# Kernel optimization log

Hardware: AMD Instinct MI355X
Metric: run time of the kernel (lower is better)

## Reference

```python
import jax, jax.numpy as jnp
import numpy as np

N_NODES = 100000
N_EDGES = 3200000
IN_FEATS = 512
HIDDEN = 256
N_CLASSES = 64
NITER = 10
HALT_BIAS_INIT = 3.0


def setup_inputs() -> dict:
    key = jax.random.key(0)
    ks = jax.random.split(key, 8)
    x = jax.random.normal(ks[0], (N_NODES, IN_FEATS), dtype=jnp.float32)
    edge_index = jax.random.randint(ks[1], (2, N_EDGES), 0, N_NODES, dtype=jnp.int64)
    # Linear layers: layers[0]: in->hidden, layers[1]: hidden->classes, halt: classes->1
    W0 = jax.random.normal(ks[2], (IN_FEATS, HIDDEN), dtype=jnp.float32) / np.sqrt(IN_FEATS)
    b0 = jnp.zeros((HIDDEN,), dtype=jnp.float32)
    W1 = jax.random.normal(ks[3], (HIDDEN, N_CLASSES), dtype=jnp.float32) / np.sqrt(HIDDEN)
    b1 = jnp.zeros((N_CLASSES,), dtype=jnp.float32)
    Wh = jax.random.normal(ks[4], (N_CLASSES, 1), dtype=jnp.float32) / np.sqrt(N_CLASSES)
    bh = jnp.full((1,), HALT_BIAS_INIT, dtype=jnp.float32)
    return {"x": x, "edge_index": edge_index, "edge_dropout": 0,
            "W0": W0, "b0": b0, "W1": W1, "b1": b1, "Wh": Wh, "bh": bh}


def reference(x, edge_index, edge_dropout, W0, b0, W1, b1, Wh, bh):
    N = x.shape[0]
    # MLP encoder (eval mode: dropout is identity)
    h = jax.nn.relu(x @ W0 + b0)
    h = h @ W1 + b1                                   # [N, C]

    # gcn_norm with self-loops (edge_dropout=0 in eval => identical every iter)
    loops = jnp.arange(N, dtype=edge_index.dtype)
    row = jnp.concatenate([edge_index[0], loops])     # source
    col = jnp.concatenate([edge_index[1], loops])     # target (aggregation index)
    deg = jax.ops.segment_sum(jnp.ones_like(col, dtype=h.dtype), col, num_segments=N)
    dinv = jnp.where(deg > 0, deg ** -0.5, 0.0)
    norm = dinv[row] * dinv[col]                      # [E+N]

    def step(ph, _):
        msg = norm[:, None] * ph[row]                 # gather + scale, [E+N, C]
        ph2 = jax.ops.segment_sum(msg, col, num_segments=N)  # scatter_add
        logit = jnp.clip(ph2 @ Wh + bh, -10.0, 10.0)  # [N, 1]
        return ph2, (ph2, logit)

    _, (props, logits) = jax.lax.scan(step, h, None, length=NITER)
    outputs = jnp.concatenate([h[None], props], axis=0)       # [niter+1, N, C]
    halting_logits = jnp.transpose(logits[:, :, 0])           # [N, niter]

    lam = jax.nn.sigmoid(halting_logits)
    remain = jnp.cumprod(1.0 - lam, axis=1)                   # inclusive
    remain_excl = jnp.concatenate([jnp.ones((N, 1), lam.dtype), remain[:, :-1]], axis=1)
    p = lam * remain_excl
    p = p.at[:, -1].add(remain[:, -1])                        # leftover mass to last step
    return outputs, p, halting_logits
```

## Files before the change

### kernel.cpp

```cpp
#include <hip/hip_runtime.h>
#include <hip/hip_bf16.h>

#define N_NODES  100000
#define N_EDGES  3200000
#define IN_FEATS 512
#define HIDDEN   256
#define N_CLASSES 64
#define NITER    10

#define SCAN_NB  49

#define OUT_P_OFF  ((size_t)(NITER + 1) * N_NODES * N_CLASSES)
#define OUT_HL_OFF (OUT_P_OFF + (size_t)N_NODES * NITER)

#define WS_META_INTS (4 * N_NODES + 128)
#define WS_CSR_OFF   ((size_t)WS_META_INTS * 4)
#define WS_W0F_OFF   (WS_CSR_OFF + (size_t)2 * N_EDGES * 4)
#define WS_W1F_OFF   (WS_W0F_OFF + 262144)
#define WS_SH0_OFF   (WS_W1F_OFF + 32768)
#define WS_SH1_OFF   (WS_SH0_OFF + (size_t)N_NODES * 64 * 2)
#define WS_NEED_W    (WS_SH0_OFF)
#define WS_NEED_BF   (WS_SH1_OFF + (size_t)N_NODES * 64 * 2)

typedef _Float16 f16x8 __attribute__((ext_vector_type(8)));
typedef _Float16 f16x4 __attribute__((ext_vector_type(4)));
typedef float    f32x4 __attribute__((ext_vector_type(4)));

__device__ __forceinline__ float bflo(unsigned v) { return __uint_as_float(v << 16); }
__device__ __forceinline__ float bfhi(unsigned v) { return __uint_as_float(v & 0xffff0000u); }
__device__ __forceinline__ unsigned short f2bf(float f) {
    unsigned u = __float_as_uint(f);
    return (unsigned short)((u + 0x7fffu + ((u >> 16) & 1u)) >> 16);
}

__global__ void k_detect(const int* ei, int* flag) {
    if (threadIdx.x == 0 && blockIdx.x == 0) {
        int is64 = 1;
        for (int k = 0; k < 128; ++k) {
            if (ei[2 * k + 1] != 0) { is64 = 0; break; }
        }
        *flag = is64;
    }
}

__device__ __forceinline__ int edge_row(const void* ei, int is64, int e) {
    return is64 ? (int)((const long long*)ei)[e] : ((const int*)ei)[e];
}
__device__ __forceinline__ int edge_col(const void* ei, int is64, int e) {
    return is64 ? (int)((const long long*)ei)[(size_t)N_EDGES + e]
                : ((const int*)ei)[(size_t)N_EDGES + e];
}

__global__ void k_count(const void* ei, const int* flag, int* cnt) {
    int e = blockIdx.x * 256 + threadIdx.x;
    if (e >= N_EDGES) return;
    int is64 = *flag;
    atomicAdd(&cnt[edge_col(ei, is64, e)], 1);
}

__global__ __launch_bounds__(256) void k_scan1(const int* cnt, int* part) {
    __shared__ int sd[256];
    int b = blockIdx.x, t = threadIdx.x;
    int s = 0;
    for (int j = t; j < 2048; j += 256) {
        int idx = b * 2048 + j;
        if (idx < N_NODES) s += cnt[idx];
    }
    sd[t] = s;
    __syncthreads();
    for (int o = 128; o > 0; o >>= 1) {
        if (t < o) sd[t] += sd[t + o];
        __syncthreads();
    }
    if (t == 0) part[b] = sd[0];
}

__global__ __launch_bounds__(256) void k_scan2(int* part, int* offs) {
    __shared__ int sd[256];
    int t = threadIdx.x;
    sd[t] = (t < SCAN_NB) ? part[t] : 0;
    __syncthreads();
    for (int o = 1; o < 256; o <<= 1) {
        int add = (t >= o) ? sd[t - o] : 0;
        __syncthreads();
        sd[t] += add;
        __syncthreads();
    }
    if (t < SCAN_NB) part[t] = (t == 0) ? 0 : sd[t - 1];
    if (t == 0) offs[N_NODES] = N_EDGES;
}

__global__ __launch_bounds__(256) void k_scan3(const int* cnt, const int* part, int* offs) {
    __shared__ int sd[256];
    int b = blockIdx.x, t = threadIdx.x;
    int base = b * 2048 + t * 8;
    int local[8];
    int s = 0;
#pragma unroll
    for (int j = 0; j < 8; ++j) {
        int idx = base + j;
        int v = (idx < N_NODES) ? cnt[idx] : 0;
        local[j] = s;
        s += v;
    }
    sd[t] = s;
    __syncthreads();
    for (int o = 1; o < 256; o <<= 1) {
        int add = (t >= o) ? sd[t - o] : 0;
        __syncthreads();
        sd[t] += add;
        __syncthreads();
    }
    int tbase = part[b] + ((t == 0) ? 0 : sd[t - 1]);
#pragma unroll
    for (int j = 0; j < 8; ++j) {
        int idx = base + j;
        if (idx < N_NODES) offs[idx] = tbase + local[j];
    }
}

__global__ void k_dinv(const int* cnt, float* dinv) {
    int i = blockIdx.x * 256 + threadIdx.x;
    if (i >= N_NODES) return;
    dinv[i] = rsqrtf((float)(cnt[i] + 1));
}

__global__ void k_fill(const void* ei, const int* flag, const float* dinv,
                       const int* offs, int* cursor, int2* csr) {
    int e = blockIdx.x * 256 + threadIdx.x;
    if (e >= N_EDGES) return;
    int is64 = *flag;
    int r = edge_row(ei, is64, e);
    int c = edge_col(ei, is64, e);
    int pos = offs[c] + atomicAdd(&cursor[c], 1);
    csr[pos] = make_int2(r, __float_as_int(dinv[r] * dinv[c]));
}

__global__ void k_prep_w(const float* __restrict__ W0, const float* __restrict__ W1,
                         _Float16* __restrict__ W0f, _Float16* __restrict__ W1f) {
    int id = blockIdx.x * 256 + threadIdx.x;
    if (id < 16384) {
        int l = id & 63, c = (id >> 6) & 15, kkg = id >> 10;
        int n = c * 16 + (l & 15);
        int kb = kkg * 32 + ((l >> 4) * 8);
        f16x8 v;
#pragma unroll
        for (int j = 0; j < 8; ++j) v[j] = (_Float16)W0[(size_t)(kb + j) * HIDDEN + n];
        *(f16x8*)&W0f[(size_t)id * 8] = v;
    } else if (id < 16384 + 2048) {
        int id2 = id - 16384;
        int l = id2 & 63, c = (id2 >> 6) & 3, kkg = id2 >> 8;
        int n = c * 16 + (l & 15);
        int kb = kkg * 32 + ((l >> 4) * 8);
        f16x8 v;
#pragma unroll
        for (int j = 0; j < 8; ++j) v[j] = (_Float16)W1[(size_t)(kb + j) * N_CLASSES + n];
        *(f16x8*)&W1f[(size_t)id2 * 8] = v;
    }
}

#define EBM 128
#define XS_STRIDE 72
#define H1_STRIDE 264
__global__ __launch_bounds__(256) void k_encoder_mfma(
        const float* __restrict__ x, const _Float16* __restrict__ W0f,
        const float* __restrict__ b0, const _Float16* __restrict__ W1f,
        const float* __restrict__ b1, float* __restrict__ out,
        unsigned short* __restrict__ shadow, int write_shadow) {
    __shared__ char smem[EBM * H1_STRIDE * 2];
    _Float16 (*xs)[XS_STRIDE]  = (_Float16(*)[XS_STRIDE])smem;
    _Float16 (*h1s)[H1_STRIDE] = (_Float16(*)[H1_STRIDE])smem;

    const int t = threadIdx.x;
    const int w = t >> 6, l = t & 63;
    const int g = l >> 4, r15 = l & 15;
    const int row0 = blockIdx.x * EBM;

    f32x4 acc[2][16];
#pragma unroll
    for (int rt = 0; rt < 2; ++rt)
#pragma unroll
        for (int c = 0; c < 16; ++c) acc[rt][c] = (f32x4){0.f, 0.f, 0.f, 0.f};

    for (int kc = 0; kc < 8; ++kc) {
        __syncthreads();
#pragma unroll
        for (int q = 0; q < 8; ++q) {
            int idx = q * 256 + t;
            int srow = idx >> 4, c4 = idx & 15;
            int grow = row0 + srow;
            if (grow >= N_NODES) grow = N_NODES - 1;
            float4 v = *(const float4*)&x[(size_t)grow * IN_FEATS + kc * 64 + c4 * 4];
            f16x4 hv = {(_Float16)v.x, (_Float16)v.y, (_Float16)v.z, (_Float16)v.w};
            *(f16x4*)&xs[srow][c4 * 4] = hv;
        }
        __syncthreads();
#pragma unroll
        for (int kk = 0; kk < 2; ++kk) {
            int kkg = kc * 2 + kk;
            f16x8 af0 = *(const f16x8*)&xs[w * 32 + r15][kk * 32 + g * 8];
            f16x8 af1 = *(const f16x8*)&xs[w * 32 + 16 + r15][kk * 32 + g * 8];
#pragma unroll
            for (int c = 0; c < 16; ++c) {
                f16x8 bf = *(const f16x8*)&W0f[(size_t)((kkg * 16 + c) * 64 + l) * 8];
                acc[0][c] = __builtin_amdgcn_mfma_f32_16x16x32_f16(af0, bf, acc[0][c], 0, 0, 0);
                acc[1][c] = __builtin_amdgcn_mfma_f32_16x16x32_f16(af1, bf, acc[1][c], 0, 0, 0);
            }
        }
    }
    __syncthreads();
#pragma unroll
    for (int c = 0; c < 16; ++c) {
        float bb = b0[c * 16 + r15];
#pragma unroll
        for (int rt = 0; rt < 2; ++rt) {
#pragma unroll
            for (int i = 0; i < 4; ++i) {
                int row = w * 32 + rt * 16 + g * 4 + i;
                h1s[row][c * 16 + r15] = (_Float16)fmaxf(acc[rt][c][i] + bb, 0.f);
            }
        }
    }
    __syncthreads();
    f32x4 acc2[2][4];
#pragma unroll
    for (int rt = 0; rt < 2; ++rt)
#pragma unroll
        for (int c = 0; c < 4; ++c) acc2[rt][c] = (f32x4){0.f, 0.f, 0.f, 0.f};
#pragma unroll
    for (int kkg = 0; kkg < 8; ++kkg) {
        f16x8 af0 = *(const f16x8*)&h1s[w * 32 + r15][kkg * 32 + g * 8];
        f16x8 af1 = *(const f16x8*)&h1s[w * 32 + 16 + r15][kkg * 32 + g * 8];
#pragma unroll
        for (int c = 0; c < 4; ++c) {
            f16x8 bf = *(const f16x8*)&W1f[(size_t)((kkg * 4 + c) * 64 + l) * 8];
            acc2[0][c] = __builtin_amdgcn_mfma_f32_16x16x32_f16(af0, bf, acc2[0][c], 0, 0, 0);
            acc2[1][c] = __builtin_amdgcn_mfma_f32_16x16x32_f16(af1, bf, acc2[1][c], 0, 0, 0);
        }
    }
#pragma unroll
    for (int c = 0; c < 4; ++c) {
        float bb = b1[c * 16 + r15];
#pragma unroll
        for (int rt = 0; rt < 2; ++rt) {
#pragma unroll
            for (int i = 0; i < 4; ++i) {
                int row = row0 + w * 32 + rt * 16 + g * 4 + i;
                if (row < N_NODES) {
                    float v = acc2[rt][c][i] + bb;
                    int col = c * 16 + r15;
                    out[(size_t)row * 64 + col] = v;
                    if (write_shadow) shadow[(size_t)row * 64 + col] = f2bf(v);
                }
            }
        }
    }
}

__global__ __launch_bounds__(256) void k_encoder(const float* __restrict__ x,
        const float* __restrict__ W0, const float* __restrict__ b0,
        const float* __restrict__ W1, const float* __restrict__ b1,
        float* __restrict__ out) {
    __shared__ float xsh[32][128];
    __shared__ float h1s[32][HIDDEN + 1];
    const int t = threadIdx.x;
    const int rg = t >> 6;
    const int cg = t & 63;
    const size_t row0 = (size_t)blockIdx.x * 32;
    float acc[8][4];
#pragma unroll
    for (int i = 0; i < 8; ++i)
        acc[i][0] = acc[i][1] = acc[i][2] = acc[i][3] = 0.f;
    for (int kc = 0; kc < 4; ++kc) {
        __syncthreads();
#pragma unroll
        for (int q = 0; q < 4; ++q) {
            int idx = t + q * 256;
            int r = idx >> 5, pos = idx & 31;
            *(float4*)&xsh[r][pos * 4] =
                *(const float4*)&x[(row0 + r) * IN_FEATS + kc * 128 + pos * 4];
        }
        __syncthreads();
        for (int kk = 0; kk < 128; kk += 4) {
            float4 xv[8];
#pragma unroll
            for (int i = 0; i < 8; ++i) xv[i] = *(const float4*)&xsh[rg * 8 + i][kk];
#pragma unroll
            for (int j = 0; j < 4; ++j) {
                float4 wv = *(const float4*)&W0[(size_t)(kc * 128 + kk + j) * HIDDEN + cg * 4];
#pragma unroll
                for (int i = 0; i < 8; ++i) {
                    float xj = (&xv[i].x)[j];
                    acc[i][0] = fmaf(xj, wv.x, acc[i][0]);
                    acc[i][1] = fmaf(xj, wv.y, acc[i][1]);
                    acc[i][2] = fmaf(xj, wv.z, acc[i][2]);
                    acc[i][3] = fmaf(xj, wv.w, acc[i][3]);
                }
            }
        }
    }
    float4 bb = *(const float4*)&b0[cg * 4];
#pragma unroll
    for (int i = 0; i < 8; ++i) {
        int r = rg * 8 + i;
        h1s[r][cg * 4 + 0] = fmaxf(acc[i][0] + bb.x, 0.f);
        h1s[r][cg * 4 + 1] = fmaxf(acc[i][1] + bb.y, 0.f);
        h1s[r][cg * 4 + 2] = fmaxf(acc[i][2] + bb.z, 0.f);
        h1s[r][cg * 4 + 3] = fmaxf(acc[i][3] + bb.w, 0.f);
    }
    __syncthreads();
    float a2[8];
#pragma unroll
    for (int i = 0; i < 8; ++i) a2[i] = 0.f;
    for (int k = 0; k < HIDDEN; ++k) {
        float wv = W1[(size_t)k * N_CLASSES + cg];
#pragma unroll
        for (int i = 0; i < 8; ++i) a2[i] = fmaf(h1s[rg * 8 + i][k], wv, a2[i]);
    }
    float bv = b1[cg];
#pragma unroll
    for (int i = 0; i < 8; ++i)
        out[(row0 + rg * 8 + i) * N_CLASSES + cg] = a2[i] + bv;
}

__global__ __launch_bounds__(256) void k_prop_bf(
        const unsigned short* __restrict__ pin_bf, float* __restrict__ pout,
        unsigned short* __restrict__ pout_bf, const int* __restrict__ offs,
        const int2* __restrict__ csr, const float* __restrict__ dinv,
        const float* __restrict__ Wh, const float* __restrict__ bh,
        float* __restrict__ hl, int t) {
    int node = (blockIdx.x * 256 + threadIdx.x) >> 5;
    if (node >= N_NODES) return;
    int hlane = threadIdx.x & 31;
    int base = threadIdx.x & 32;
    float di = dinv[node];
    unsigned vs = *(const unsigned*)&pin_bf[(size_t)node * 64 + hlane * 2];
    float a0 = di * di * bflo(vs), a1 = di * di * bfhi(vs);
    float c0 = 0.f, c1 = 0.f;
    int e0 = offs[node], e1 = offs[node + 1];
    for (int eb = e0; eb < e1; eb += 32) {
        int n = e1 - eb; if (n > 32) n = 32;
        int idx = eb + hlane;
        int2 ew = csr[idx < e1 ? idx : e1 - 1];
        int j = 0;
        for (; j + 8 <= n; j += 8) {
            unsigned v[8]; float w[8];
#pragma unroll
            for (int q = 0; q < 8; ++q) {
                int s = __shfl(ew.x, base + j + q, 64);
                w[q] = __int_as_float(__shfl(ew.y, base + j + q, 64));
                v[q] = *(const unsigned*)&pin_bf[(size_t)s * 64 + hlane * 2];
            }
#pragma unroll
            for (int q = 0; q < 8; ++q) {
                if (q & 1) { c0 = fmaf(w[q], bflo(v[q]), c0); c1 = fmaf(w[q], bfhi(v[q]), c1); }
                else       { a0 = fmaf(w[q], bflo(v[q]), a0); a1 = fmaf(w[q], bfhi(v[q]), a1); }
            }
        }
        for (; j < n; ++j) {
            int s = __shfl(ew.x, base + j, 64);
            float w = __int_as_float(__shfl(ew.y, base + j, 64));
            unsigned v = *(const unsigned*)&pin_bf[(size_t)s * 64 + hlane * 2];
            a0 = fmaf(w, bflo(v), a0);
            a1 = fmaf(w, bfhi(v), a1);
        }
    }
    float fa = a0 + c0, fb = a1 + c1;
    *(float2*)&pout[(size_t)node * 64 + hlane * 2] = make_float2(fa, fb);
    *(unsigned*)&pout_bf[(size_t)node * 64 + hlane * 2] =
        (unsigned)f2bf(fa) | ((unsigned)f2bf(fb) << 16);
    float2 wh = *(const float2*)&Wh[hlane * 2];
    float s = fa * wh.x + fb * wh.y;
#pragma unroll
    for (int o = 16; o > 0; o >>= 1) s += __shfl_xor(s, o, 64);
    if (hlane == 0) {
        float lg = s + bh[0];
        lg = fminf(10.0f, fmaxf(-10.0f, lg));
        hl[(size_t)node * NITER + t] = lg;
    }
}

__global__ __launch_bounds__(256) void k_prop(const float* __restrict__ pin,
        float* __restrict__ pout, const int* __restrict__ offs,
        const int2* __restrict__ csr, const float* __restrict__ dinv,
        const float* __restrict__ Wh, const float* __restrict__ bh,
        float* __restrict__ hl, int t) {
    int wid = (blockIdx.x * blockDim.x + threadIdx.x) >> 6;
    int lane = threadIdx.x & 63;
    if (wid >= N_NODES) return;
    float di = dinv[wid];
    float a[4];
    a[0] = di * di * pin[(size_t)wid * 64 + lane];
    a[1] = a[2] = a[3] = 0.f;
    int e0 = offs[wid], e1 = offs[wid + 1];
    for (int eb = e0; eb < e1; eb += 64) {
        int n = e1 - eb; if (n > 64) n = 64;
        int idx = eb + lane;
        int2 ew = csr[idx < e1 ? idx : e1 - 1];
        int j = 0;
        for (; j + 8 <= n; j += 8) {
            float v[8], w[8];
#pragma unroll
            for (int q = 0; q < 8; ++q) {
                int s = __shfl(ew.x, j + q, 64);
                w[q] = __int_as_float(__shfl(ew.y, j + q, 64));
                v[q] = pin[(size_t)s * 64 + lane];
            }
#pragma unroll
            for (int q = 0; q < 8; ++q) a[q & 3] = fmaf(w[q], v[q], a[q & 3]);
        }
        for (; j < n; ++j) {
            int s = __shfl(ew.x, j, 64);
            float w = __int_as_float(__shfl(ew.y, j, 64));
            a[0] = fmaf(w, pin[(size_t)s * 64 + lane], a[0]);
        }
    }
    float acc = (a[0] + a[1]) + (a[2] + a[3]);
    pout[(size_t)wid * 64 + lane] = acc;
    float s = acc * Wh[lane];
#pragma unroll
    for (int o = 32; o > 0; o >>= 1) s += __shfl_xor(s, o, 64);
    if (lane == 0) {
        float lg = s + bh[0];
        lg = fminf(10.0f, fmaxf(-10.0f, lg));
        hl[(size_t)wid * NITER + t] = lg;
    }
}

__global__ void k_p(const float* __restrict__ hl, float* __restrict__ p) {
    int i = blockIdx.x * 256 + threadIdx.x;
    if (i >= N_NODES) return;
    float remain = 1.0f;
    float pv[NITER];
#pragma unroll
    for (int t = 0; t < NITER; ++t) {
        float lg = hl[(size_t)i * NITER + t];
        float lam = 1.0f / (1.0f + expf(-lg));
        pv[t] = lam * remain;
        remain *= (1.0f - lam);
    }
    pv[NITER - 1] += remain;
#pragma unroll
    for (int t = 0; t < NITER; ++t) p[(size_t)i * NITER + t] = pv[t];
}

extern "C" void kernel_launch(void* const* d_in, const int* in_sizes, int n_in,
                              void* d_out, int out_size, void* d_ws, size_t ws_size,
                              hipStream_t stream) {
    const float* x  = (const float*)d_in[0];
    const void*  ei = d_in[1];
    const float* W0 = (const float*)d_in[3];
    const float* b0 = (const float*)d_in[4];
    const float* W1 = (const float*)d_in[5];
    const float* b1 = (const float*)d_in[6];
    const float* Wh = (const float*)d_in[7];
    const float* bh = (const float*)d_in[8];
    float* out = (float*)d_out;

    int* ws_i   = (int*)d_ws;
    int* cnt    = ws_i;
    int* offs   = ws_i + N_NODES;
    int* cursor = ws_i + 2 * N_NODES + 2;
    int* part   = ws_i + 3 * N_NODES + 2;
    int* flag   = ws_i + 3 * N_NODES + 66;
    float* dinv = (float*)(ws_i + 3 * N_NODES + 128);
    int2* csr   = (int2*)((char*)d_ws + WS_CSR_OFF);
    _Float16* W0f = (_Float16*)((char*)d_ws + WS_W0F_OFF);
    _Float16* W1f = (_Float16*)((char*)d_ws + WS_W1F_OFF);
    unsigned short* sh0 = (unsigned short*)((char*)d_ws + WS_SH0_OFF);
    unsigned short* sh1 = (unsigned short*)((char*)d_ws + WS_SH1_OFF);

    const int use_w  = ws_size >= WS_NEED_W;
    const int use_bf = ws_size >= WS_NEED_BF;

    hipMemsetAsync(d_ws, 0, (size_t)(3 * N_NODES + 128) * 4, stream);
    k_detect<<<1, 64, 0, stream>>>((const int*)ei, flag);
    k_count<<<(N_EDGES + 255) / 256, 256, 0, stream>>>(ei, flag, cnt);
    k_scan1<<<SCAN_NB, 256, 0, stream>>>(cnt, part);
    k_scan2<<<1, 256, 0, stream>>>(part, offs);
    k_scan3<<<SCAN_NB, 256, 0, stream>>>(cnt, part, offs);
    k_dinv<<<(N_NODES + 255) / 256, 256, 0, stream>>>(cnt, dinv);
    k_fill<<<(N_EDGES + 255) / 256, 256, 0, stream>>>(ei, flag, dinv, offs, cursor, csr);

    if (use_w) {
        k_prep_w<<<72, 256, 0, stream>>>(W0, W1, W0f, W1f);
        k_encoder_mfma<<<(N_NODES + EBM - 1) / EBM, 256, 0, stream>>>(
            x, W0f, b0, W1f, b1, out, sh0, use_bf);
    } else {
        k_encoder<<<N_NODES / 32, 256, 0, stream>>>(x, W0, b0, W1, b1, out);
    }

    float* hl = out + OUT_HL_OFF;
    if (use_bf) {
        for (int it = 0; it < NITER; ++it) {
            const unsigned short* pin_bf = (it & 1) ? sh1 : sh0;
            unsigned short* pout_bf      = (it & 1) ? sh0 : sh1;
            float* pout = out + (size_t)(it + 1) * N_NODES * N_CLASSES;
            k_prop_bf<<<((size_t)N_NODES * 32 + 255) / 256, 256, 0, stream>>>(
                pin_bf, pout, pout_bf, offs, csr, dinv, Wh, bh, hl, it);
        }
    } else {
        for (int it = 0; it < NITER; ++it) {
            const float* pin = out + (size_t)it * N_NODES * N_CLASSES;
            float* pout      = out + (size_t)(it + 1) * N_NODES * N_CLASSES;
            k_prop<<<((size_t)N_NODES * 64 + 255) / 256, 256, 0, stream>>>(
                pin, pout, offs, csr, dinv, Wh, bh, hl, it);
        }
    }
    k_p<<<(N_NODES + 255) / 256, 256, 0, stream>>>(hl, out + OUT_P_OFF);
}
```

Measured before the change: 1.151 ms.

## Double-buffer encoder x tiles with register prefetch and halve row tile

The MFMA encoder now processes 64 rows per block instead of 128, with each wave owning one 16-row tile. It prefetches the next 64-column chunk of x into registers while the current chunk is multiplied, and uses two LDS buffers so each k-step needs one barrier instead of two. The goal is to hide global-load latency behind MFMA work and to raise occupancy through lower accumulator register pressure and more blocks. The cost is that W0f/W1f fragments are reused across fewer rows, which raises weight-load traffic per output row.

After: 1.175 ms. 2.2% more time.

```diff
diff --git a/kernel.cpp b/kernel.cpp
--- a/kernel.cpp
+++ b/kernel.cpp
@@ -159,7 +159,7 @@
     }
 }
 
-#define EBM 128
+#define EBM 64
 #define XS_STRIDE 72
 #define H1_STRIDE 264
 __global__ __launch_bounds__(256) void k_encoder_mfma(
@@ -168,43 +168,62 @@
         const float* __restrict__ b1, float* __restrict__ out,
         unsigned short* __restrict__ shadow, int write_shadow) {
     __shared__ char smem[EBM * H1_STRIDE * 2];
-    _Float16 (*xs)[XS_STRIDE]  = (_Float16(*)[XS_STRIDE])smem;
     _Float16 (*h1s)[H1_STRIDE] = (_Float16(*)[H1_STRIDE])smem;
+    _Float16 (*xsb[2])[XS_STRIDE];
+    xsb[0] = (_Float16(*)[XS_STRIDE])smem;
+    xsb[1] = (_Float16(*)[XS_STRIDE])(smem + EBM * XS_STRIDE * 2);
 
     const int t = threadIdx.x;
     const int w = t >> 6, l = t & 63;
     const int g = l >> 4, r15 = l & 15;
     const int row0 = blockIdx.x * EBM;
-
-    f32x4 acc[2][16];
-#pragma unroll
-    for (int rt = 0; rt < 2; ++rt)
-#pragma unroll
-        for (int c = 0; c < 16; ++c) acc[rt][c] = (f32x4){0.f, 0.f, 0.f, 0.f};
+    const int srow[4] = {(0 * 256 + t) >> 4, (1 * 256 + t) >> 4,
+                         (2 * 256 + t) >> 4, (3 * 256 + t) >> 4};
+    const int c4 = t & 15;
+
+    f32x4 acc[16];
+#pragma unroll
+    for (int c = 0; c < 16; ++c) acc[c] = (f32x4){0.f, 0.f, 0.f, 0.f};
+
+    float4 ld[4];
+#pragma unroll
+    for (int q = 0; q < 4; ++q) {
+        int grow = row0 + srow[q];
+        if (grow >= N_NODES) grow = N_NODES - 1;
+        ld[q] = *(const float4*)&x[(size_t)grow * IN_FEATS + c4 * 4];
+    }
+#pragma unroll
+    for (int q = 0; q < 4; ++q) {
+        f16x4 hv = {(_Float16)ld[q].x, (_Float16)ld[q].y, (_Float16)ld[q].z, (_Float16)ld[q].w};
+        *(f16x4*)&xsb[0][srow[q]][c4 * 4] = hv;
+    }
 
     for (int kc = 0; kc < 8; ++kc) {
-        __syncthreads();
-#pragma unroll
-        for (int q = 0; q < 8; ++q) {
-            int idx = q * 256 + t;
-            int srow = idx >> 4, c4 = idx & 15;
-            int grow = row0 + srow;
-            if (grow >= N_NODES) grow = N_NODES - 1;
-            float4 v = *(const float4*)&x[(size_t)grow * IN_FEATS + kc * 64 + c4 * 4];
-            f16x4 hv = {(_Float16)v.x, (_Float16)v.y, (_Float16)v.z, (_Float16)v.w};
-            *(f16x4*)&xs[srow][c4 * 4] = hv;
-        }
-        __syncthreads();
+        if (kc < 7) {
+#pragma unroll
+            for (int q = 0; q < 4; ++q) {
+                int grow = row0 + srow[q];
+                if (grow >= N_NODES) grow = N_NODES - 1;
+                ld[q] = *(const float4*)&x[(size_t)grow * IN_FEATS + (kc + 1) * 64 + c4 * 4];
+            }
+        }
+        __syncthreads();
+        _Float16 (*xs)[XS_STRIDE] = xsb[kc & 1];
 #pragma unroll
         for (int kk = 0; kk < 2; ++kk) {
             int kkg = kc * 2 + kk;
-            f16x8 af0 = *(const f16x8*)&xs[w * 32 + r15][kk * 32 + g * 8];
-            f16x8 af1 = *(const f16x8*)&xs[w * 32 + 16 + r15][kk * 32 + g * 8];
+            f16x8 af = *(const f16x8*)&xs[w * 16 + r15][kk * 32 + g * 8];
 #pragma unroll
             for (int c = 0; c < 16; ++c) {
                 f16x8 bf = *(const f16x8*)&W0f[(size_t)((kkg * 16 + c) * 64 + l) * 8];
-                acc[0][c] = __builtin_amdgcn_mfma_f32_16x16x32_f16(af0, bf, acc[0][c], 0, 0, 0);
-                acc[1][c] = __builtin_amdgcn_mfma_f32_16x16x32_f16(af1, bf, acc[1][c], 0, 0, 0);
+                acc[c] = __builtin_amdgcn_mfma_f32_16x16x32_f16(af, bf, acc[c], 0, 0, 0);
+            }
+        }
+        if (kc < 7) {
+#pragma unroll
+            for (int q = 0; q < 4; ++q) {
+                f16x4 hv = {(_Float16)ld[q].x, (_Float16)ld[q].y, (_Float16)ld[q].z, (_Float16)ld[q].w};
+                *(f16x4*)&xsb[(kc + 1) & 1][srow[q]][c4 * 4] = hv;
             }
         }
     }
@@ -213,45 +232,35 @@
     for (int c = 0; c < 16; ++c) {
         float bb = b0[c * 16 + r15];
 #pragma unroll
-        for (int rt = 0; rt < 2; ++rt) {
-#pragma unroll
-            for (int i = 0; i < 4; ++i) {
-                int row = w * 32 + rt * 16 + g * 4 + i;
-                h1s[row][c * 16 + r15] = (_Float16)fmaxf(acc[rt][c][i] + bb, 0.f);
-            }
+        for (int i = 0; i < 4; ++i) {
+            int row = w * 16 + g * 4 + i;
+            h1s[row][c * 16 + r15] = (_Float16)fmaxf(acc[c][i] + bb, 0.f);
         }
     }
     __syncthreads();
-    f32x4 acc2[2][4];
-#pragma unroll
-    for (int rt = 0; rt < 2; ++rt)
-#pragma unroll
-        for (int c = 0; c < 4; ++c) acc2[rt][c] = (f32x4){0.f, 0.f, 0.f, 0.f};
+    f32x4 acc2[4];
+#pragma unroll
+    for (int c = 0; c < 4; ++c) acc2[c] = (f32x4){0.f, 0.f, 0.f, 0.f};
 #pragma unroll
     for (int kkg = 0; kkg < 8; ++kkg) {
-        f16x8 af0 = *(const f16x8*)&h1s[w * 32 + r15][kkg * 32 + g * 8];
-        f16x8 af1 = *(const f16x8*)&h1s[w * 32 + 16 + r15][kkg * 32 + g * 8];
+        f16x8 af = *(const f16x8*)&h1s[w * 16 + r15][kkg * 32 + g * 8];
 #pragma unroll
         for (int c = 0; c < 4; ++c) {
             f16x8 bf = *(const f16x8*)&W1f[(size_t)((kkg * 4 + c) * 64 + l) * 8];
-            acc2[0][c] = __builtin_amdgcn_mfma_f32_16x16x32_f16(af0, bf, acc2[0][c], 0, 0, 0);
-            acc2[1][c] = __builtin_amdgcn_mfma_f32_16x16x32_f16(af1, bf, acc2[1][c], 0, 0, 0);
+            acc2[c] = __builtin_amdgcn_mfma_f32_16x16x32_f16(af, bf, acc2[c], 0, 0, 0);
         }
     }
 #pragma unroll
     for (int c = 0; c < 4; ++c) {
         float bb = b1[c * 16 + r15];
 #pragma unroll
-        for (int rt = 0; rt < 2; ++rt) {
-#pragma unroll
-            for (int i = 0; i < 4; ++i) {
-                int row = row0 + w * 32 + rt * 16 + g * 4 + i;
-                if (row < N_NODES) {
-                    float v = acc2[rt][c][i] + bb;
-                    int col = c * 16 + r15;
-                    out[(size_t)row * 64 + col] = v;
-                    if (write_shadow) shadow[(size_t)row * 64 + col] = f2bf(v);
-                }
+        for (int i = 0; i < 4; ++i) {
+            int row = row0 + w * 16 + g * 4 + i;
+            if (row < N_NODES) {
+                float v = acc2[c][i] + bb;
+                int col = c * 16 + r15;
+                out[(size_t)row * 64 + col] = v;
+                if (write_shadow) shadow[(size_t)row * 64 + col] = f2bf(v);
             }
         }
     }
```
